# Optimization experiments

Hardware: AMD Instinct MI355X
Metric: run time of the kernel (lower is better)

The kernel has to match this reference:

```python
import jax, jax.numpy as jnp
import numpy as np

VOCAB = 32000
DEPTH = 18
INNER = VOCAB - 1
EPS = 1e-9


def setup_inputs() -> dict:
    key = jax.random.key(0)
    k_att, k_w, k_idx, k_sign = jax.random.split(key, 4)
    B, T, D = 4, 16, 512
    att = jax.random.normal(k_att, (B, T, D), dtype=jnp.float32)
    # nn.Linear weight, scaled like kaiming-uniform-ish
    W = jax.random.normal(k_w, (INNER, D), dtype=jnp.float32) * (1.0 / np.sqrt(D))
    n = VOCAB * DEPTH
    path_index = jax.random.randint(k_idx, (n,), 0, INNER, dtype=jnp.int32)
    # Huffman path signs: +1 (left child) or -1 (right child)
    path_sign = jnp.where(jax.random.uniform(k_sign, (n,)) < 0.5, 1.0, -1.0).astype(jnp.float32)
    # bias so that prob = sigmoid(h) for left, 1 - sigmoid(h) for right
    path_bias = (1.0 - path_sign) * 0.5
    return {"att": att, "W": W, "path_index": path_index,
            "path_sign": path_sign, "path_bias": path_bias}


def reference(att, W, path_index, path_sign, path_bias):
    B, T, _ = att.shape
    # Linear (no bias) + sigmoid: [B, T, INNER]
    h = jax.nn.sigmoid(jnp.einsum('btd,nd->btn', att, W))
    # gather along inner-node axis to per-(vocab, depth) path probs
    g = jnp.take(h, path_index, axis=-1) * path_sign + path_bias  # [B, T, VOCAB*DEPTH]
    H = g.reshape(B, T, VOCAB, DEPTH)
    H = jnp.clip(H, EPS, 1.0 - EPS)
    logp = jnp.sum(jnp.log(H), axis=-1)  # [B, T, VOCAB]
    return logp
```

## Files before the change

### kernel.cpp

```cpp
#include <hip/hip_runtime.h>
#include <hip/hip_bf16.h>

#define INNER 31999
#define VOCAB 32000
#define DEPTH 18
#define M_DIM 64
#define K_DIM 512
#define LDS_K (K_DIM + 8)

typedef __attribute__((ext_vector_type(8))) short bf16x8;
typedef __attribute__((ext_vector_type(4))) short s16x4;
typedef __attribute__((ext_vector_type(4))) float f32x4;
typedef __attribute__((ext_vector_type(2))) _Float16 f16x2;

__device__ __forceinline__ unsigned int pkbf(float a, float b) {
    const unsigned int ua = __float_as_uint(a) + 0x8000u;
    const unsigned int ub = __float_as_uint(b) + 0x8000u;
    return __builtin_amdgcn_perm(ub, ua, 0x07060302u);
}

__device__ __forceinline__ bf16x8 cvt8(f32x4 lo, f32x4 hi) {
    union { unsigned int u[4]; bf16x8 v; } r;
    r.u[0] = pkbf(lo[0], lo[1]);
    r.u[1] = pkbf(lo[2], lo[3]);
    r.u[2] = pkbf(hi[0], hi[1]);
    r.u[3] = pkbf(hi[2], hi[3]);
    return r.v;
}

__global__ __launch_bounds__(256) void gemm_xt_kernel(
    const float* __restrict__ W,
    const float* __restrict__ att,
    _Float16* __restrict__ xT)
{
    __shared__ __align__(16) unsigned short attb[M_DIM * LDS_K];

    const int tid  = threadIdx.x;
    const int wave = tid >> 6;
    const int lane = tid & 63;
    const int mrow = lane & 15;
    const int quad = lane >> 4;

    #pragma unroll
    for (int i = 0; i < 32; i++) {
        const int f4 = i * 256 + tid;
        const f32x4 v = ((const f32x4*)att)[f4];
        const int f = f4 * 4;
        const int m = f >> 9, k = f & (K_DIM - 1);
        union { unsigned int u[2]; s16x4 s; } o;
        o.u[0] = pkbf(v[0], v[1]);
        o.u[1] = pkbf(v[2], v[3]);
        *(s16x4*)(attb + m * LDS_K + k) = o.s;
    }
    __syncthreads();

    const int n_base = blockIdx.x * 64 + wave * 16;
    const int n = n_base + mrow;
    const int nc = n < INNER ? n : (INNER - 1);
    const float* wp = W + (size_t)nc * K_DIM;

    f32x4 acc[4];
    #pragma unroll
    for (int j = 0; j < 4; j++) acc[j] = (f32x4){0.f, 0.f, 0.f, 0.f};

    #pragma unroll
    for (int k0i = 0; k0i < 16; k0i++) {
        const int koff = k0i * 32 + quad * 8;
        const f32x4* p = (const f32x4*)(wp + koff);
        const bf16x8 a = cvt8(p[0], p[1]);
        #pragma unroll
        for (int j = 0; j < 4; j++) {
            const bf16x8 b = *(const bf16x8*)(attb + (j * 16 + mrow) * LDS_K + koff);
            acc[j] = __builtin_amdgcn_mfma_f32_16x16x32_bf16(a, b, acc[j], 0, 0, 0);
        }
    }

    #pragma unroll
    for (int j = 0; j < 4; j++) {
        const int m = j * 16 + mrow;
        #pragma unroll
        for (int r = 0; r < 4; r++)
            xT[(size_t)(n_base + quad * 4 + r) * M_DIM + m] = (_Float16)acc[j][r];
    }
}

__global__ __launch_bounds__(256) void hsoftmax_kernel(
    const _Float16* __restrict__ xT,
    const int*   __restrict__ path_index,
    const float* __restrict__ path_sign,
    float* __restrict__ out)
{
    __shared__ unsigned int packed[32 * DEPTH];
    __shared__ float2 res2[32][33];

    const int tid = threadIdx.x;
    const int wave = tid >> 6;
    const int lane = tid & 63;
    const int half = lane >> 5;
    const int sub  = lane & 31;
    const int v_base = blockIdx.x * 32;
    const int base = v_base * DEPTH;

    for (int t = tid; t < 32 * DEPTH; t += 256) {
        const unsigned int idx = (unsigned int)path_index[base + t];
        const float s = path_sign[base + t];
        packed[t] = idx | (s < 0.f ? 0x80000000u : 0u);
    }
    __syncthreads();

    for (int i = 0; i < 4; i++) {
        const int vloc = wave * 8 + 2 * i + half;
        float accmin0 = 0.f, accmin1 = 0.f;
        float prod0 = 1.f, prod1 = 1.f;
        #pragma unroll
        for (int d = 0; d < DEPTH; d++) {
            const unsigned int p = packed[vloc * DEPTH + d];
            const unsigned int xx = *(const unsigned int*)(
                (const unsigned short*)xT + (p & 0x7fffu) * M_DIM + sub * 2);
            union { unsigned int u; f16x2 h; } cv; cv.u = xx;
            const float x0 = (float)cv.h[0];
            const float x1 = (float)cv.h[1];
            const unsigned int sgn = p & 0x80000000u;
            const unsigned int xb0 = __float_as_uint(x0);
            const unsigned int xb1 = __float_as_uint(x1);
            const float e0 = __expf(__uint_as_float(xb0 | 0x80000000u));
            const float e1 = __expf(__uint_as_float(xb1 | 0x80000000u));
            prod0 = fmaf(prod0, e0, prod0);
            prod1 = fmaf(prod1, e1, prod1);
            accmin0 += fminf(__uint_as_float(xb0 ^ sgn), 0.f);
            accmin1 += fminf(__uint_as_float(xb1 ^ sgn), 0.f);
        }
        const float r0 = fmaxf(accmin0 - __logf(prod0), -373.1f);
        const float r1 = fmaxf(accmin1 - __logf(prod1), -373.1f);
        res2[vloc][sub] = make_float2(r0, r1);
    }
    __syncthreads();

    #pragma unroll
    for (int it = 0; it < 8; it++) {
        const int m = it * 8 + (tid >> 5);
        const int vloc = tid & 31;
        out[(size_t)m * VOCAB + v_base + vloc] = ((const float*)&res2[vloc][0])[m];
    }
}

extern "C" void kernel_launch(void* const* d_in, const int* in_sizes, int n_in,
                              void* d_out, int out_size, void* d_ws, size_t ws_size,
                              hipStream_t stream) {
    const float* att        = (const float*)d_in[0];
    const float* W          = (const float*)d_in[1];
    const int*   path_index = (const int*)d_in[2];
    const float* path_sign  = (const float*)d_in[3];

    _Float16* xT = (_Float16*)d_ws;
    float* out = (float*)d_out;

    gemm_xt_kernel<<<500, 256, 0, stream>>>(W, att, xT);
    hsoftmax_kernel<<<1000, 256, 0, stream>>>(xT, path_index, path_sign, out);
}
```

Measured before the change: 122.1 us.

## Precompute clamped log-sigmoid tables in GEMM epilogue and sum them in gather

```diff
diff --git a/kernel.cpp b/kernel.cpp
--- a/kernel.cpp
+++ b/kernel.cpp
@@ -7,6 +7,9 @@
 #define M_DIM 64
 #define K_DIM 512
 #define LDS_K (K_DIM + 8)
+
+#define LM_BYTE_OFF 4194304u
+#define LOG_EPS -20.723265f
 
 typedef __attribute__((ext_vector_type(8))) short bf16x8;
 typedef __attribute__((ext_vector_type(4))) short s16x4;
@@ -28,10 +31,11 @@
     return r.v;
 }
 
-__global__ __launch_bounds__(256) void gemm_xt_kernel(
+__global__ __launch_bounds__(256) void gemm_ls_kernel(
     const float* __restrict__ W,
     const float* __restrict__ att,
-    _Float16* __restrict__ xT)
+    _Float16* __restrict__ Lp,
+    _Float16* __restrict__ Lm)
 {
     __shared__ __align__(16) unsigned short attb[M_DIM * LDS_K];
 
@@ -63,29 +67,47 @@
     #pragma unroll
     for (int j = 0; j < 4; j++) acc[j] = (f32x4){0.f, 0.f, 0.f, 0.f};
 
+    int koff = quad * 8;
+    f32x4 wa = *(const f32x4*)(wp + koff);
+    f32x4 wb = *(const f32x4*)(wp + koff + 4);
     #pragma unroll
     for (int k0i = 0; k0i < 16; k0i++) {
-        const int koff = k0i * 32 + quad * 8;
-        const f32x4* p = (const f32x4*)(wp + koff);
-        const bf16x8 a = cvt8(p[0], p[1]);
+        f32x4 na, nb;
+        if (k0i < 15) {
+            na = *(const f32x4*)(wp + koff + 32);
+            nb = *(const f32x4*)(wp + koff + 36);
+        }
+        const bf16x8 a = cvt8(wa, wb);
         #pragma unroll
         for (int j = 0; j < 4; j++) {
             const bf16x8 b = *(const bf16x8*)(attb + (j * 16 + mrow) * LDS_K + koff);
             acc[j] = __builtin_amdgcn_mfma_f32_16x16x32_bf16(a, b, acc[j], 0, 0, 0);
         }
+        wa = na; wb = nb;
+        koff += 32;
     }
 
     #pragma unroll
     for (int j = 0; j < 4; j++) {
         const int m = j * 16 + mrow;
         #pragma unroll
-        for (int r = 0; r < 4; r++)
-            xT[(size_t)(n_base + quad * 4 + r) * M_DIM + m] = (_Float16)acc[j][r];
+        for (int r = 0; r < 4; r++) {
+            const float x = acc[j][r];
+            const float e = __expf(-fabsf(x));
+            const float L = __logf(1.0f + e);
+            float lsp = fminf(x, 0.f) - L;
+            float lsm = lsp - x;
+            lsp = fmaxf(lsp, LOG_EPS);
+            lsm = fmaxf(lsm, LOG_EPS);
+            const size_t row = (size_t)(n_base + quad * 4 + r) * M_DIM;
+            Lp[row + m] = (_Float16)lsp;
+            Lm[row + m] = (_Float16)lsm;
+        }
     }
 }
 
 __global__ __launch_bounds__(256) void hsoftmax_kernel(
-    const _Float16* __restrict__ xT,
+    const char*  __restrict__ tab,
     const int*   __restrict__ path_index,
     const float* __restrict__ path_sign,
     float* __restrict__ out)
@@ -104,35 +126,23 @@
     for (int t = tid; t < 32 * DEPTH; t += 256) {
         const unsigned int idx = (unsigned int)path_index[base + t];
         const float s = path_sign[base + t];
-        packed[t] = idx | (s < 0.f ? 0x80000000u : 0u);
+        packed[t] = (idx << 7) + (s < 0.f ? LM_BYTE_OFF : 0u);
     }
     __syncthreads();
 
+    const int boff = sub * 4;
     for (int i = 0; i < 4; i++) {
         const int vloc = wave * 8 + 2 * i + half;
-        float accmin0 = 0.f, accmin1 = 0.f;
-        float prod0 = 1.f, prod1 = 1.f;
+        float a0 = 0.f, a1 = 0.f;
         #pragma unroll
         for (int d = 0; d < DEPTH; d++) {
-            const unsigned int p = packed[vloc * DEPTH + d];
-            const unsigned int xx = *(const unsigned int*)(
-                (const unsigned short*)xT + (p & 0x7fffu) * M_DIM + sub * 2);
+            const unsigned int off = packed[vloc * DEPTH + d];
+            const unsigned int xx = *(const unsigned int*)(tab + off + boff);
             union { unsigned int u; f16x2 h; } cv; cv.u = xx;
-            const float x0 = (float)cv.h[0];
-            const float x1 = (float)cv.h[1];
-            const unsigned int sgn = p & 0x80000000u;
-            const unsigned int xb0 = __float_as_uint(x0);
-            const unsigned int xb1 = __float_as_uint(x1);
-            const float e0 = __expf(__uint_as_float(xb0 | 0x80000000u));
-            const float e1 = __expf(__uint_as_float(xb1 | 0x80000000u));
-            prod0 = fmaf(prod0, e0, prod0);
-            prod1 = fmaf(prod1, e1, prod1);
-            accmin0 += fminf(__uint_as_float(xb0 ^ sgn), 0.f);
-            accmin1 += fminf(__uint_as_float(xb1 ^ sgn), 0.f);
+            a0 += (float)cv.h[0];
+            a1 += (float)cv.h[1];
         }
-        const float r0 = fmaxf(accmin0 - __logf(prod0), -373.1f);
-        const float r1 = fmaxf(accmin1 - __logf(prod1), -373.1f);
-        res2[vloc][sub] = make_float2(r0, r1);
+        res2[vloc][sub] = make_float2(a0, a1);
     }
     __syncthreads();
 
@@ -152,9 +162,10 @@
     const int*   path_index = (const int*)d_in[2];
     const float* path_sign  = (const float*)d_in[3];
 
-    _Float16* xT = (_Float16*)d_ws;
+    _Float16* Lp = (_Float16*)d_ws;
+    _Float16* Lm = (_Float16*)((char*)d_ws + LM_BYTE_OFF);
     float* out = (float*)d_out;
 
-    gemm_xt_kernel<<<500, 256, 0, stream>>>(W, att, xT);
-    hsoftmax_kernel<<<1000, 256, 0, stream>>>(xT, path_index, path_sign, out);
+    gemm_ls_kernel<<<500, 256, 0, stream>>>(W, att, Lp, Lm);
+    hsoftmax_kernel<<<1000, 256, 0, stream>>>((const char*)Lp, path_index, path_sign, out);
 }
```

Result: faster. 117.4 us (-3.8%).
